# Performance work log

Hardware: AMD Instinct MI355X
Metric: run time of the kernel (lower is better)

## Reference

```python
import jax, jax.numpy as jnp
import numpy as np


def setup_inputs() -> dict:
    key = jax.random.key(0)
    ks = jax.random.split(key, 7)
    B, T, I, H, O = 64, 2048, 32, 256, 32
    s = 0.05
    return {
        "x": jax.random.normal(ks[0], (B, T, I), dtype=jnp.float32),
        "W_ih": jax.random.normal(ks[1], (4 * H, I), dtype=jnp.float32) * s,
        "W_hh": jax.random.normal(ks[2], (4 * H, H), dtype=jnp.float32) * s,
        "b_ih": jax.random.normal(ks[3], (4 * H,), dtype=jnp.float32) * s,
        "b_hh": jax.random.normal(ks[4], (4 * H,), dtype=jnp.float32) * s,
        "fc_w": jax.random.normal(ks[5], (O, H), dtype=jnp.float32) * s,
        "fc_b": jax.random.normal(ks[6], (O,), dtype=jnp.float32) * s,
    }


def _lstm(x, W_ih, W_hh, b_ih, b_hh):
    # x: [B,T,I]; PyTorch gate order: i, f, g, o stacked along 4H axis.
    B = x.shape[0]
    H = W_hh.shape[1]
    # Precompute input contributions for all timesteps in one GEMM: [B,T,4H]
    xg = jnp.einsum('bti,gi->btg', x, W_ih) + b_ih + b_hh

    def step(carry, xg_t):
        h, c = carry  # [B,H] each
        gates = xg_t + h @ W_hh.T  # [B,4H]
        i, f, g, o = jnp.split(gates, 4, axis=-1)
        i = jax.nn.sigmoid(i)
        f = jax.nn.sigmoid(f)
        g = jnp.tanh(g)
        o = jax.nn.sigmoid(o)
        c = f * c + i * g
        h = o * jnp.tanh(c)
        return (h, c), h

    h0 = jnp.zeros((B, H), dtype=x.dtype)
    (_, _), hs = jax.lax.scan(step, (h0, h0), jnp.swapaxes(xg, 0, 1))
    return jnp.swapaxes(hs, 0, 1)  # [B,T,H]


def reference(x, W_ih, W_hh, b_ih, b_hh, fc_w, fc_b):
    out = _lstm(x, W_ih, W_hh, b_ih, b_hh)          # [B,T,H]
    # Conv1d(H, O, kernel_size=1) over channel dim == pointwise linear.
    return jnp.einsum('bth,oh->bto', out, fc_w) + fc_b  # [B,T,O]
```

## Files before the change

kernel.cpp:

```cpp
#include <hip/hip_runtime.h>
#include <cstdint>


#define B_  64
#define T_  2048
#define I_  32
#define H_  256
#define G4  1024
#define O_  32

typedef int v16i __attribute__((ext_vector_type(16)));
typedef int v4i  __attribute__((ext_vector_type(4)));
typedef _Float16 h2_t __attribute__((ext_vector_type(2)));

#if __has_builtin(__builtin_amdgcn_sdot4)
__device__ __forceinline__ int dot4(int a, int b, int c) {
    return __builtin_amdgcn_sdot4(a, b, c, false);
}
#else
__device__ __forceinline__ int dot4(int a, int b, int c) {
    c += (int)(int8_t)(a)        * (int)(int8_t)(b);
    c += (int)(int8_t)(a >> 8)   * (int)(int8_t)(b >> 8);
    c += (int)(int8_t)(a >> 16)  * (int)(int8_t)(b >> 16);
    c += (int)(int8_t)(a >> 24)  * (int)(int8_t)(b >> 24);
    return c;
}
#endif

__device__ __forceinline__ float fdot2h(h2_t a, h2_t b, float c) {
#if __has_builtin(__builtin_amdgcn_fdot2)
    return __builtin_amdgcn_fdot2(a, b, c, false);
#else
    return c + (float)a[0] * (float)b[0] + (float)a[1] * (float)b[1];
#endif
}

#define QWHH_OFF 0
#define QWIH_OFF 262144
#define S1_OFF   327680
#define S2_OFF   331776
#define BIAS_OFF 335872
#define XQ_OFF   339968
#define XS_OFF   8728576
#define HBUF_OFF 9252864
#define HREC_STRIDE 320
#define HSLOTS 2049

__device__ __forceinline__ uint32_t pack_q(int q0, int q1, int q2, int q3) {
    return  ((uint32_t)(uint8_t)(int8_t)q0)
          | (((uint32_t)(uint8_t)(int8_t)q1) << 8)
          | (((uint32_t)(uint8_t)(int8_t)q2) << 16)
          | (((uint32_t)(uint8_t)(int8_t)q3) << 24);
}

__device__ __forceinline__ int clamp127(int v) {
    return v < -127 ? -127 : (v > 127 ? 127 : v);
}

__global__ __launch_bounds__(64) void prep_w(
    const float* __restrict__ Whh, const float* __restrict__ Wih,
    const float* __restrict__ bih, const float* __restrict__ bhh,
    uint32_t* __restrict__ qwhh, uint32_t* __restrict__ qwih,
    float* __restrict__ s1, float* __restrict__ s2, float* __restrict__ bias)
{
    const int r = blockIdx.x;
    const int l = threadIdx.x;

    const float4 wv = ((const float4*)(Whh + r * H_))[l];
    float m = fmaxf(fmaxf(fabsf(wv.x), fabsf(wv.y)), fmaxf(fabsf(wv.z), fabsf(wv.w)));
    #pragma unroll
    for (int s = 1; s < 64; s <<= 1) m = fmaxf(m, __shfl_xor(m, s, 64));
    const float S1 = fmaxf(m, 1e-20f) / 127.f;

    float xm = (l < I_) ? fabsf(Wih[r * I_ + l]) : 0.f;
    #pragma unroll
    for (int s = 1; s < 64; s <<= 1) xm = fmaxf(xm, __shfl_xor(xm, s, 64));
    const float S2 = fmaxf(xm, 1e-20f) / 127.f;

    {
        const float r1 = 1.f / S1;
        qwhh[l * G4 + r] = pack_q(
            clamp127((int)rintf(wv.x * r1)), clamp127((int)rintf(wv.y * r1)),
            clamp127((int)rintf(wv.z * r1)), clamp127((int)rintf(wv.w * r1)));
    }
    if (l < 8) {
        const float4 xw = ((const float4*)(Wih + r * I_))[l];
        const float r2 = 1.f / S2;
        qwih[l * G4 + r] = pack_q(
            clamp127((int)rintf(xw.x * r2)), clamp127((int)rintf(xw.y * r2)),
            clamp127((int)rintf(xw.z * r2)), clamp127((int)rintf(xw.w * r2)));
    } else if (l < 16) {
        const int j = l - 8;
        const float4 xw = ((const float4*)(Wih + r * I_))[j];
        const float r2 = 1.f / S2;
        float v0 = xw.x * r2, v1 = xw.y * r2, v2 = xw.z * r2, v3 = xw.w * r2;
        int a0 = clamp127((int)rintf(v0)), a1 = clamp127((int)rintf(v1));
        int a2 = clamp127((int)rintf(v2)), a3 = clamp127((int)rintf(v3));
        qwih[(8 + j) * G4 + r] = pack_q(
            clamp127((int)rintf((v0 - (float)a0) * 127.f)),
            clamp127((int)rintf((v1 - (float)a1) * 127.f)),
            clamp127((int)rintf((v2 - (float)a2) * 127.f)),
            clamp127((int)rintf((v3 - (float)a3) * 127.f)));
    }
    if (l == 0) { s1[r] = S1; s2[r] = S2; bias[r] = bih[r] + bhh[r]; }
}

__global__ __launch_bounds__(256) void prep_x(
    const float* __restrict__ x, uint32_t* __restrict__ xq, float* __restrict__ xs)
{
    __shared__ float xb[64 * 32];
    const int base = blockIdx.x * 64 * 32;
    for (int i = threadIdx.x; i < 2048; i += 256) xb[i] = x[base + i];
    __syncthreads();
    const int t = threadIdx.x;
    if (t < 64) {
        float m = 0.f;
        for (int k = 0; k < 32; k++) m = fmaxf(m, fabsf(xb[t * 32 + k]));
        const float S = fmaxf(m, 1e-20f) / 127.f;
        const int row = blockIdx.x * 64 + t;
        xs[row] = S;
        const float rS = 1.f / S;
        for (int j = 0; j < 8; j++) {
            int qa[4], qb[4];
            for (int e = 0; e < 4; e++) {
                float v = xb[t * 32 + j * 4 + e] * rS;
                int a = clamp127((int)rintf(v));
                int b = clamp127((int)rintf((v - (float)a) * 127.f));
                qa[e] = a; qb[e] = b;
            }
            xq[row * 16 + j]     = pack_q(qa[0], qa[1], qa[2], qa[3]);
            xq[row * 16 + 8 + j] = pack_q(qb[0], qb[1], qb[2], qb[3]);
        }
    }
}

__device__ __forceinline__ float x_contrib(const uint32_t* pxq, const float* pxs,
                                           const uint32_t* wA, const uint32_t* wB,
                                           float S2, float bias_r) {
    v16i xv; int sxi;
    asm volatile("s_load_dwordx16 %0, %2, 0x0\n\t"
                 "s_load_dword %1, %3, 0x0\n\t"
                 "s_waitcnt lgkmcnt(0)"
                 : "=&s"(xv), "=&s"(sxi)
                 : "s"(pxq), "s"(pxs)
                 : "memory");
    int aA = 0, aM = 0;
    #pragma unroll
    for (int j = 0; j < 8; j++) {
        aA = dot4((int)wA[j], xv[j],     aA);
        aM = dot4((int)wA[j], xv[8 + j], aM);
        aM = dot4((int)wB[j], xv[j],     aM);
    }
    return ((float)aA + (float)aM * (1.f / 127.f)) * (S2 * __int_as_float(sxi)) + bias_r;
}

__global__ __launch_bounds__(1024, 4) void lstm_main(
    const uint32_t* __restrict__ qwhh, const uint32_t* __restrict__ qwih,
    const float* __restrict__ s1v, const float* __restrict__ s2v,
    const float* __restrict__ biasv,
    const uint32_t* __restrict__ xq, const float* __restrict__ xs,
    const float* __restrict__ fcw, const float* __restrict__ fcb,
    char* __restrict__ hbuf, float* __restrict__ out)
{
    const int b   = blockIdx.x;
    const int tid = threadIdx.x;

    __shared__ float    gbuf[768];
    __shared__ uint32_t hf16[128];

    uint32_t w[64], wA[8], wB[8];
    #pragma unroll
    for (int d = 0; d < 64; d++) w[d] = qwhh[d * G4 + tid];
    #pragma unroll
    for (int j = 0; j < 8; j++) { wA[j] = qwih[j * G4 + tid]; wB[j] = qwih[(8 + j) * G4 + tid]; }
    const float S1 = s1v[tid], S2 = s2v[tid], bias_r = biasv[tid];

    const int o_ = tid >> 5, kc = tid & 31;
    h2_t fw[4];
    {
        const float* fr = fcw + o_ * H_ + kc * 8;
        #pragma unroll
        for (int j = 0; j < 4; j++) {
            h2_t p; p[0] = (_Float16)fr[2 * j]; p[1] = (_Float16)fr[2 * j + 1];
            fw[j] = p;
        }
    }
    const float fcb_v = fcb[o_];

    char* hb = hbuf + (size_t)b * (HSLOTS * HREC_STRIDE);
    if (tid < H_) hb[2048 * HREC_STRIDE + tid] = 0;
    if (tid >= 256 && tid < 260) ((float*)(hb + 2048 * HREC_STRIDE + 256))[tid - 256] = 0.f;

    const uint32_t* xqb  = xq + (size_t)(b * T_) * 16;
    const float*    xsb  = xs + (size_t)(b * T_);
    float*          outb = out + (size_t)(b * T_) * O_;

    float c_state = 0.f;
    float x_part  = x_contrib(xqb, xsb, wA, wB, S2, bias_r);

    __syncthreads();

    for (int t = 0; t < T_; t++) {
        const uint32_t slot = (t == 0) ? 2048u : ((uint32_t)(t * 1993) & 2047u);
        const char* hrec = hb + (size_t)slot * HREC_STRIDE;
        v16i h0, h1, h2, h3; v4i scv;
        asm volatile("s_load_dwordx16 %0, %5, 0x0\n\t"
                     "s_load_dwordx16 %1, %5, 0x40\n\t"
                     "s_load_dwordx16 %2, %5, 0x80\n\t"
                     "s_load_dwordx16 %3, %5, 0xc0\n\t"
                     "s_load_dwordx4  %4, %5, 0x100\n\t"
                     "s_waitcnt lgkmcnt(0)"
                     : "=&s"(h0), "=&s"(h1), "=&s"(h2), "=&s"(h3), "=&s"(scv)
                     : "s"(hrec)
                     : "memory");

        int a0 = 0, a1 = 0, a2 = 0, a3 = 0;
        #pragma unroll
        for (int d = 0; d < 16; d++) {
            a0 = dot4((int)w[d],      h0[d], a0);
            a1 = dot4((int)w[16 + d], h1[d], a1);
            a2 = dot4((int)w[32 + d], h2[d], a2);
            a3 = dot4((int)w[48 + d], h3[d], a3);
        }
        const float hsum = (float)a0 * __int_as_float(scv[0])
                         + (float)a1 * __int_as_float(scv[1])
                         + (float)a2 * __int_as_float(scv[2])
                         + (float)a3 * __int_as_float(scv[3]);
        const float gate = hsum * S1 + x_part;

        if (tid >= 256) gbuf[tid - 256] = gate;
        __syncthreads();

        const uint32_t wslot = (uint32_t)((t + 1) * 1993) & 2047u;
        char* hw = hb + (size_t)wslot * HREC_STRIDE;
        float hval = 0.f;
        if (tid < H_) {
            const float gi = gate;
            const float gf = gbuf[tid];
            const float gg = gbuf[256 + tid];
            const float go = gbuf[512 + tid];
            const float i_ = 1.f / (1.f + __expf(-gi));
            const float f_ = 1.f / (1.f + __expf(-gf));
            const float g_ = 2.f / (1.f + __expf(-2.f * gg)) - 1.f;
            const float oo = 1.f / (1.f + __expf(-go));
            c_state = f_ * c_state + i_ * g_;
            const float tc = 2.f / (1.f + __expf(-2.f * c_state)) - 1.f;
            hval = oo * tc;
            ((_Float16*)hf16)[tid] = (_Float16)hval;

            float m = fabsf(hval);
            #pragma unroll
            for (int s = 1; s < 64; s <<= 1) m = fmaxf(m, __shfl_xor(m, s, 64));
            m = fmaxf(m, 1e-12f);
            const float rq = 127.f / m;
            const int q = clamp127((int)rintf(hval * rq));
            hw[tid] = (char)(int8_t)q;
            if ((tid & 63) == 0)
                ((float*)(hw + 256))[tid >> 6] = m * (1.f / 127.f);
        }

        if (t < T_ - 1)
            x_part = x_contrib(xqb + (size_t)(t + 1) * 16, xsb + (t + 1),
                               wA, wB, S2, bias_r);

        __syncthreads();

        {
            const uint4 hv = *(const uint4*)(&hf16[4 * kc]);
            union { uint32_t u; h2_t h; } u0, u1, u2, u3;
            u0.u = hv.x; u1.u = hv.y; u2.u = hv.z; u3.u = hv.w;
            float acc = 0.f;
            acc = fdot2h(fw[0], u0.h, acc);
            acc = fdot2h(fw[1], u1.h, acc);
            acc = fdot2h(fw[2], u2.h, acc);
            acc = fdot2h(fw[3], u3.h, acc);
            #pragma unroll
            for (int s = 1; s < 32; s <<= 1) acc += __shfl_xor(acc, s, 64);
            if (kc == 0) outb[t * O_ + o_] = acc + fcb_v;
        }
    }
}

extern "C" void kernel_launch(void* const* d_in, const int* in_sizes, int n_in,
                              void* d_out, int out_size, void* d_ws, size_t ws_size,
                              hipStream_t stream) {
    const float* x    = (const float*)d_in[0];
    const float* Wih  = (const float*)d_in[1];
    const float* Whh  = (const float*)d_in[2];
    const float* bih  = (const float*)d_in[3];
    const float* bhh  = (const float*)d_in[4];
    const float* fcw  = (const float*)d_in[5];
    const float* fcb  = (const float*)d_in[6];
    float* out = (float*)d_out;

    char* ws = (char*)d_ws;
    uint32_t* qwhh = (uint32_t*)(ws + QWHH_OFF);
    uint32_t* qwih = (uint32_t*)(ws + QWIH_OFF);
    float*    s1   = (float*)(ws + S1_OFF);
    float*    s2   = (float*)(ws + S2_OFF);
    float*    bias = (float*)(ws + BIAS_OFF);
    uint32_t* xq   = (uint32_t*)(ws + XQ_OFF);
    float*    xs   = (float*)(ws + XS_OFF);
    char*     hbuf = ws + HBUF_OFF;

    prep_w<<<G4, 64, 0, stream>>>(Whh, Wih, bih, bhh, qwhh, qwih, s1, s2, bias);
    prep_x<<<(B_ * T_) / 64, 256, 0, stream>>>(x, xq, xs);
    lstm_main<<<B_, 1024, 0, stream>>>(qwhh, qwih, s1, s2, bias, xq, xs,
                                       fcw, fcb, hbuf, out);
}
```

Baseline: 3.528 ms.

## Overlap FC output and x prefetch with h scalar loads; use DPP reductions

Moves the fc projection of the previous step's hidden state into the window while the scalar loads of the current h record are in flight. It also issues the next timestep's x-input loads as vector loads there, separating the s_waitcnt from the load asm. Shuffle-based max and sum reductions are replaced with DPP row/broadcast sequences plus readlane. This shortens the serial per-step critical path, at the cost of a step-skewed output write and a peeled epilogue for the last timestep.

```diff
diff --git a/kernel.cpp b/kernel.cpp
--- a/kernel.cpp
+++ b/kernel.cpp
@@ -11,6 +11,7 @@
 
 typedef int v16i __attribute__((ext_vector_type(16)));
 typedef int v4i  __attribute__((ext_vector_type(4)));
+typedef unsigned int v4u __attribute__((ext_vector_type(4)));
 typedef _Float16 h2_t __attribute__((ext_vector_type(2)));
 
 #if __has_builtin(__builtin_amdgcn_sdot4)
@@ -33,6 +34,33 @@
 #else
     return c + (float)a[0] * (float)b[0] + (float)a[1] * (float)b[1];
 #endif
+}
+
+__device__ __forceinline__ float wave64_max_bcast(float v) {
+    int t;
+    t = __builtin_amdgcn_update_dpp(__float_as_int(v), __float_as_int(v), 0x111, 0xf, 0xf, false);
+    v = fmaxf(v, __int_as_float(t));
+    t = __builtin_amdgcn_update_dpp(__float_as_int(v), __float_as_int(v), 0x112, 0xf, 0xf, false);
+    v = fmaxf(v, __int_as_float(t));
+    t = __builtin_amdgcn_update_dpp(__float_as_int(v), __float_as_int(v), 0x114, 0xf, 0xf, false);
+    v = fmaxf(v, __int_as_float(t));
+    t = __builtin_amdgcn_update_dpp(__float_as_int(v), __float_as_int(v), 0x118, 0xf, 0xf, false);
+    v = fmaxf(v, __int_as_float(t));
+    t = __builtin_amdgcn_update_dpp(__float_as_int(v), __float_as_int(v), 0x142, 0xa, 0xf, false);
+    v = fmaxf(v, __int_as_float(t));
+    t = __builtin_amdgcn_update_dpp(__float_as_int(v), __float_as_int(v), 0x143, 0xc, 0xf, false);
+    v = fmaxf(v, __int_as_float(t));
+    return __int_as_float(__builtin_amdgcn_readlane(__float_as_int(v), 63));
+}
+
+__device__ __forceinline__ float halfwave_sum31(float v) {
+    int t;
+    t = __builtin_amdgcn_update_dpp(0, __float_as_int(v), 0x111, 0xf, 0xf, true); v += __int_as_float(t);
+    t = __builtin_amdgcn_update_dpp(0, __float_as_int(v), 0x112, 0xf, 0xf, true); v += __int_as_float(t);
+    t = __builtin_amdgcn_update_dpp(0, __float_as_int(v), 0x114, 0xf, 0xf, true); v += __int_as_float(t);
+    t = __builtin_amdgcn_update_dpp(0, __float_as_int(v), 0x118, 0xf, 0xf, true); v += __int_as_float(t);
+    t = __builtin_amdgcn_update_dpp(0, __float_as_int(v), 0x142, 0xa, 0xf, true); v += __int_as_float(t);
+    return v;
 }
 
 #define QWHH_OFF 0
@@ -134,24 +162,20 @@
     }
 }
 
-__device__ __forceinline__ float x_contrib(const uint32_t* pxq, const float* pxs,
-                                           const uint32_t* wA, const uint32_t* wB,
-                                           float S2, float bias_r) {
-    v16i xv; int sxi;
-    asm volatile("s_load_dwordx16 %0, %2, 0x0\n\t"
-                 "s_load_dword %1, %3, 0x0\n\t"
-                 "s_waitcnt lgkmcnt(0)"
-                 : "=&s"(xv), "=&s"(sxi)
-                 : "s"(pxq), "s"(pxs)
-                 : "memory");
+__device__ __forceinline__ float xdots(v4u x0, v4u x1, v4u x2, v4u x3, float sx,
+                                       const uint32_t* wA, const uint32_t* wB,
+                                       float S2, float bias_r) {
     int aA = 0, aM = 0;
     #pragma unroll
-    for (int j = 0; j < 8; j++) {
-        aA = dot4((int)wA[j], xv[j],     aA);
-        aM = dot4((int)wA[j], xv[8 + j], aM);
-        aM = dot4((int)wB[j], xv[j],     aM);
-    }
-    return ((float)aA + (float)aM * (1.f / 127.f)) * (S2 * __int_as_float(sxi)) + bias_r;
+    for (int j = 0; j < 4; j++) {
+        aA = dot4((int)wA[j],     (int)x0[j], aA);
+        aM = dot4((int)wA[j],     (int)x2[j], aM);
+        aM = dot4((int)wB[j],     (int)x0[j], aM);
+        aA = dot4((int)wA[4 + j], (int)x1[j], aA);
+        aM = dot4((int)wA[4 + j], (int)x3[j], aM);
+        aM = dot4((int)wB[4 + j], (int)x1[j], aM);
+    }
+    return ((float)aA + (float)aM * (1.f / 127.f)) * (S2 * sx) + bias_r;
 }
 
 __global__ __launch_bounds__(1024, 4) void lstm_main(
@@ -196,7 +220,12 @@
     float*          outb = out + (size_t)(b * T_) * O_;
 
     float c_state = 0.f;
-    float x_part  = x_contrib(xqb, xsb, wA, wB, S2, bias_r);
+    float x_part;
+    {
+        const v4u x0 = *(const v4u*)(xqb);     const v4u x1 = *(const v4u*)(xqb + 4);
+        const v4u x2 = *(const v4u*)(xqb + 8); const v4u x3 = *(const v4u*)(xqb + 12);
+        x_part = xdots(x0, x1, x2, x3, xsb[0], wA, wB, S2, bias_r);
+    }
 
     __syncthreads();
 
@@ -208,10 +237,33 @@
                      "s_load_dwordx16 %1, %5, 0x40\n\t"
                      "s_load_dwordx16 %2, %5, 0x80\n\t"
                      "s_load_dwordx16 %3, %5, 0xc0\n\t"
-                     "s_load_dwordx4  %4, %5, 0x100\n\t"
-                     "s_waitcnt lgkmcnt(0)"
+                     "s_load_dwordx4  %4, %5, 0x100"
                      : "=&s"(h0), "=&s"(h1), "=&s"(h2), "=&s"(h3), "=&s"(scv)
                      : "s"(hrec)
+                     : "memory");
+
+        const int tn = (t + 1 < T_) ? (t + 1) : t;
+        const uint32_t* px = xqb + (size_t)tn * 16;
+        const v4u x0 = *(const v4u*)(px);     const v4u x1 = *(const v4u*)(px + 4);
+        const v4u x2 = *(const v4u*)(px + 8); const v4u x3 = *(const v4u*)(px + 12);
+        const float sx = xsb[tn];
+
+        if (t > 0) {
+            const v4u hv = *(const v4u*)(&hf16[4 * kc]);
+            union { uint32_t u; h2_t h; } u0, u1, u2, u3;
+            u0.u = hv[0]; u1.u = hv[1]; u2.u = hv[2]; u3.u = hv[3];
+            float acc = 0.f;
+            acc = fdot2h(fw[0], u0.h, acc);
+            acc = fdot2h(fw[1], u1.h, acc);
+            acc = fdot2h(fw[2], u2.h, acc);
+            acc = fdot2h(fw[3], u3.h, acc);
+            acc = halfwave_sum31(acc);
+            if ((tid & 31) == 31) outb[(t - 1) * O_ + o_] = acc + fcb_v;
+        }
+
+        asm volatile("s_waitcnt lgkmcnt(0)"
+                     : "+s"(h0), "+s"(h1), "+s"(h2), "+s"(h3), "+s"(scv)
+                     :
                      : "memory");
 
         int a0 = 0, a1 = 0, a2 = 0, a3 = 0;
@@ -233,7 +285,6 @@
 
         const uint32_t wslot = (uint32_t)((t + 1) * 1993) & 2047u;
         char* hw = hb + (size_t)wslot * HREC_STRIDE;
-        float hval = 0.f;
         if (tid < H_) {
             const float gi = gate;
             const float gf = gbuf[tid];
@@ -245,12 +296,10 @@
             const float oo = 1.f / (1.f + __expf(-go));
             c_state = f_ * c_state + i_ * g_;
             const float tc = 2.f / (1.f + __expf(-2.f * c_state)) - 1.f;
-            hval = oo * tc;
+            const float hval = oo * tc;
             ((_Float16*)hf16)[tid] = (_Float16)hval;
 
-            float m = fabsf(hval);
-            #pragma unroll
-            for (int s = 1; s < 64; s <<= 1) m = fmaxf(m, __shfl_xor(m, s, 64));
+            float m = wave64_max_bcast(fabsf(hval));
             m = fmaxf(m, 1e-12f);
             const float rq = 127.f / m;
             const int q = clamp127((int)rintf(hval * rq));
@@ -259,25 +308,22 @@
                 ((float*)(hw + 256))[tid >> 6] = m * (1.f / 127.f);
         }
 
-        if (t < T_ - 1)
-            x_part = x_contrib(xqb + (size_t)(t + 1) * 16, xsb + (t + 1),
-                               wA, wB, S2, bias_r);
+        x_part = xdots(x0, x1, x2, x3, sx, wA, wB, S2, bias_r);
 
         __syncthreads();
-
-        {
-            const uint4 hv = *(const uint4*)(&hf16[4 * kc]);
-            union { uint32_t u; h2_t h; } u0, u1, u2, u3;
-            u0.u = hv.x; u1.u = hv.y; u2.u = hv.z; u3.u = hv.w;
-            float acc = 0.f;
-            acc = fdot2h(fw[0], u0.h, acc);
-            acc = fdot2h(fw[1], u1.h, acc);
-            acc = fdot2h(fw[2], u2.h, acc);
-            acc = fdot2h(fw[3], u3.h, acc);
-            #pragma unroll
-            for (int s = 1; s < 32; s <<= 1) acc += __shfl_xor(acc, s, 64);
-            if (kc == 0) outb[t * O_ + o_] = acc + fcb_v;
-        }
+    }
+
+    {
+        const v4u hv = *(const v4u*)(&hf16[4 * kc]);
+        union { uint32_t u; h2_t h; } u0, u1, u2, u3;
+        u0.u = hv[0]; u1.u = hv[1]; u2.u = hv[2]; u3.u = hv[3];
+        float acc = 0.f;
+        acc = fdot2h(fw[0], u0.h, acc);
+        acc = fdot2h(fw[1], u1.h, acc);
+        acc = fdot2h(fw[2], u2.h, acc);
+        acc = fdot2h(fw[3], u3.h, acc);
+        acc = halfwave_sum31(acc);
+        if ((tid & 31) == 31) outb[(T_ - 1) * O_ + o_] = acc + fcb_v;
     }
 }
 
```

New measurement: 3.711 ms. +5.2%, slower.
